# Kernel tuning notes

Hardware: AMD Instinct MI355X
Metric: run time of the kernel (lower is better)

## Reference

```python
import jax, jax.numpy as jnp
import numpy as np

EPS = 1e-6
ROPE_THETA = 10000.0


def rms_norm(x, w):
    # x: [..., hd]
    var = jnp.mean(x * x, axis=-1, keepdims=True)
    return x * jax.lax.rsqrt(var + EPS) * w


def apply_rope(x):
    # x: [B, L, nH, hd], rotate-half RoPE over sequence positions
    B, L, nH, hd = x.shape
    half = hd // 2
    inv_freq = 1.0 / (ROPE_THETA ** (jnp.arange(half, dtype=jnp.float32) / half))
    pos = jnp.arange(L, dtype=jnp.float32)
    freqs = pos[:, None] * inv_freq[None, :]          # [L, half]
    cos = jnp.cos(freqs)[None, :, None, :]            # [1, L, 1, half]
    sin = jnp.sin(freqs)[None, :, None, :]
    x1, x2 = x[..., :half], x[..., half:]
    return jnp.concatenate([x1 * cos - x2 * sin, x1 * sin + x2 * cos], axis=-1)


def setup_inputs() -> dict:
    key = jax.random.key(0)
    ks = jax.random.split(key, 5)
    B, H, W, C = 2, 48, 48, 512
    nH, nKV = 8, 4
    hd = C // nH
    s = 0.02
    return {
        "x": jax.random.normal(ks[0], (B, H, W, C), jnp.float32),
        "wq": jax.random.normal(ks[1], (C, C), jnp.float32) * s,
        "wk": jax.random.normal(ks[2], (C, nKV * hd), jnp.float32) * s,
        "wv": jax.random.normal(ks[3], (C, nKV * hd), jnp.float32) * s,
        "wo": jax.random.normal(ks[4], (C, C), jnp.float32) * s,
        "q_norm_w": jnp.ones((hd,), jnp.float32),
        "k_norm_w": jnp.ones((hd,), jnp.float32),
    }


def reference(x, wq, wk, wv, wo, q_norm_w, k_norm_w):
    B, H, W, C = x.shape
    L = H * W
    nH = 8
    hd = C // nH
    nKV = wk.shape[-1] // hd

    xf = x.reshape(B, L, C)
    q = (xf @ wq).reshape(B, L, nH, hd)
    k = (xf @ wk).reshape(B, L, nKV, hd)
    v = (xf @ wv).reshape(B, L, nKV, hd)

    q = apply_rope(rms_norm(q, q_norm_w))
    k = apply_rope(rms_norm(k, k_norm_w))

    q = q.transpose(0, 2, 1, 3)                       # [B, nH, L, hd]
    k = k.transpose(0, 2, 1, 3)                       # [B, nKV, L, hd]
    v = v.transpose(0, 2, 1, 3)
    if nKV < nH:
        rep = nH // nKV
        k = jnp.repeat(k, rep, axis=1)                # repeat_interleave over heads
        v = jnp.repeat(v, rep, axis=1)

    scale = 1.0 / jnp.sqrt(jnp.array(hd, jnp.float32))
    scores = jnp.einsum("bhqd,bhkd->bhqk", q, k) * scale
    attn = jax.nn.softmax(scores, axis=-1)
    out = jnp.einsum("bhqk,bhkd->bhqd", attn, v)      # [B, nH, L, hd]
    out = out.transpose(0, 2, 1, 3).reshape(B, H, W, C)
    return out @ wo
```

## Files before the change

### kernel.cpp

```cpp
#include <hip/hip_runtime.h>
#include <cstdint>
#include <cmath>

typedef float    f32x4  __attribute__((ext_vector_type(4)));
typedef uint32_t u32x4  __attribute__((ext_vector_type(4)));
typedef uint16_t u16x8  __attribute__((ext_vector_type(8)));
typedef __bf16   bf16x8 __attribute__((ext_vector_type(8)));

#define DEVI __device__ __forceinline__

#if __has_builtin(__builtin_amdgcn_exp2f)
DEVI float fast_exp2(float x) { return __builtin_amdgcn_exp2f(x); }
#else
DEVI float fast_exp2(float x) { return exp2f(x); }
#endif

constexpr int L   = 2304;
constexpr int C   = 512;
constexpr int NH  = 8;
constexpr int NKV = 4;
constexpr int HD  = 64;
constexpr int Bn  = 2;
constexpr int M   = Bn * L;
constexpr int NQKV = C + 2 * NKV * HD;
constexpr int NSPLIT = 4;
constexpr int KTILES = 36 / NSPLIT;

constexpr int LDA = 40;
constexpr int LDP = 72;

DEVI uint16_t f2bf(float f) {
  union { float f; uint32_t u; } v; v.f = f;
  uint32_t u = v.u;
  return (uint16_t)((u + 0x7fffu + ((u >> 16) & 1u)) >> 16);
}
DEVI float bf2f(uint16_t h) {
  union { uint32_t u; float f; } v; v.u = ((uint32_t)h) << 16;
  return v.f;
}
DEVI uint16_t f2h(float f) {
  _Float16 h = (_Float16)f;
  return __builtin_bit_cast(uint16_t, h);
}
DEVI float h2f(uint16_t u) {
  return (float)__builtin_bit_cast(_Float16, u);
}

DEVI bool detect_fp32(const void* qw_raw) {
  return ((const uint16_t*)qw_raw)[0] == 0;
}

DEVI f32x4 mfma_bf16(u32x4 a, u32x4 b, f32x4 c) {
  return __builtin_amdgcn_mfma_f32_16x16x32_bf16(
      __builtin_bit_cast(bf16x8, a), __builtin_bit_cast(bf16x8, b), c, 0, 0, 0);
}

DEVI void gld16(const void* g, void* l) {
  __builtin_amdgcn_global_load_lds((const __attribute__((address_space(1))) void*)g,
                                   (__attribute__((address_space(3))) void*)l,
                                   16, 0, 0);
}

__global__ __launch_bounds__(256) void k_prep(
    const void* __restrict__ x,
    const void* __restrict__ wq, const void* __restrict__ wk,
    const void* __restrict__ wv, const void* __restrict__ wo,
    const void* __restrict__ qw_raw,
    uint16_t* __restrict__ xb,
    uint16_t* __restrict__ wqkvT, uint16_t* __restrict__ woT) {
  const bool f32 = detect_fp32(qw_raw);
  const int bi = blockIdx.x;
  const int t = threadIdx.x;
  if (bi >= 192) {
    const int i = ((bi - 192) * 256 + t) * 8;
    if (f32) {
      const float* xf = (const float*)x;
      const f32x4 v0 = *(const f32x4*)&xf[i];
      const f32x4 v1 = *(const f32x4*)&xf[i + 4];
      u16x8 o;
#pragma unroll
      for (int j = 0; j < 4; ++j) { o[j] = f2bf(v0[j]); o[j + 4] = f2bf(v1[j]); }
      *(u16x8*)&xb[i] = o;
    } else {
      *(u16x8*)&xb[i] = *(const u16x8*)((const uint16_t*)x + i);
    }
    return;
  }
  __shared__ uint16_t tile[64][72];
  const void* src; uint16_t* dst;
  int src_ld, col0, n0, k0;
  if (bi < 128) {
    const int nt = bi & 15, kt = bi >> 4;
    n0 = nt * 64; k0 = kt * 64;
    if (n0 < 512)      { src = wq; src_ld = 512; col0 = n0; }
    else if (n0 < 768) { src = wk; src_ld = 256; col0 = n0 - 512; }
    else               { src = wv; src_ld = 256; col0 = n0 - 768; }
    dst = wqkvT + n0 * 512 + k0;
  } else {
    const int bi2 = bi - 128;
    const int nt = bi2 & 7, kt = bi2 >> 3;
    n0 = nt * 64; k0 = kt * 64;
    src = wo; src_ld = 512; col0 = n0;
    dst = woT + n0 * 512 + k0;
  }
  const int rr = t >> 2, c4 = t & 3;
  if (f32) {
    const float* s32 = (const float*)src;
    for (int cc = c4; cc < 8; cc += 4) {
      const f32x4 v0 = *(const f32x4*)&s32[(k0 + rr) * src_ld + col0 + cc * 8];
      const f32x4 v1 = *(const f32x4*)&s32[(k0 + rr) * src_ld + col0 + cc * 8 + 4];
      for (int j = 0; j < 4; ++j) {
        tile[rr][cc * 8 + j]     = f2bf(v0[j]);
        tile[rr][cc * 8 + j + 4] = f2bf(v1[j]);
      }
    }
  } else {
    const uint16_t* s16 = (const uint16_t*)src;
    for (int cc = c4; cc < 8; cc += 4) {
      const u16x8 v = *(const u16x8*)&s16[(k0 + rr) * src_ld + col0 + cc * 8];
      for (int j = 0; j < 8; ++j) tile[rr][cc * 8 + j] = v[j];
    }
  }
  __syncthreads();
  for (int cc = c4; cc < 8; cc += 4) {
    u16x8 o;
    for (int j = 0; j < 8; ++j) o[j] = tile[cc * 8 + j][rr];
    *(u16x8*)&dst[rr * 512 + cc * 8] = o;
  }
}

DEVI void gemm128_core(const uint16_t* __restrict__ A, const uint16_t* __restrict__ Bt,
                       int m0, int n0, uint16_t* As, uint16_t* Bs, f32x4 acc[4][4]) {
  const int t = threadIdx.x;
  const int lane = t & 63, wave = t >> 6;
  const int l15 = lane & 15, quad = lane >> 4;
  const int wm = wave >> 1, wn = wave & 1;
#pragma unroll
  for (int i = 0; i < 4; ++i)
#pragma unroll
    for (int j = 0; j < 4; ++j) acc[i][j] = f32x4{0.f, 0.f, 0.f, 0.f};

  const int r0 = t >> 2, c0 = t & 3;

  for (int k0 = 0; k0 < C; k0 += 32) {
    const u16x8 a0 = *(const u16x8*)&A [(m0 + r0)      * C + k0 + c0 * 8];
    const u16x8 a1 = *(const u16x8*)&A [(m0 + r0 + 64) * C + k0 + c0 * 8];
    const u16x8 b0 = *(const u16x8*)&Bt[(n0 + r0)      * C + k0 + c0 * 8];
    const u16x8 b1 = *(const u16x8*)&Bt[(n0 + r0 + 64) * C + k0 + c0 * 8];
    __syncthreads();
    *(u16x8*)&As[r0 * LDA + c0 * 8]        = a0;
    *(u16x8*)&As[(r0 + 64) * LDA + c0 * 8] = a1;
    *(u16x8*)&Bs[r0 * LDA + c0 * 8]        = b0;
    *(u16x8*)&Bs[(r0 + 64) * LDA + c0 * 8] = b1;
    __syncthreads();
    u32x4 af[4], bf[4];
#pragma unroll
    for (int mt = 0; mt < 4; ++mt)
      af[mt] = *(const u32x4*)&As[(wm * 64 + mt * 16 + l15) * LDA + quad * 8];
#pragma unroll
    for (int nt = 0; nt < 4; ++nt)
      bf[nt] = *(const u32x4*)&Bs[(wn * 64 + nt * 16 + l15) * LDA + quad * 8];
#pragma unroll
    for (int mt = 0; mt < 4; ++mt)
#pragma unroll
      for (int nt = 0; nt < 4; ++nt)
        acc[mt][nt] = mfma_bf16(af[mt], bf[nt], acc[mt][nt]);
  }
}

__global__ __launch_bounds__(256, 2) void k_gemm_qkv(
    const uint16_t* __restrict__ xb, const uint16_t* __restrict__ wqkvT,
    uint16_t* __restrict__ q_p, uint16_t* __restrict__ k_p, uint16_t* __restrict__ v_t,
    const void* __restrict__ qw_raw, const void* __restrict__ kw_raw) {
  __shared__ uint16_t As[128 * LDA], Bs[128 * LDA];
  const bool f32 = detect_fp32(qw_raw);
  const int m0 = blockIdx.x * 128, n0 = blockIdx.y * 128;
  f32x4 acc[4][4];
  gemm128_core(xb, wqkvT, m0, n0, As, Bs, acc);
  const int t = threadIdx.x, lane = t & 63, wave = t >> 6;
  const int l15 = lane & 15, quad = lane >> 4;
  const int wm = wave >> 1, wn = wave & 1;
  const int col0 = n0 + wn * 64;

  if (col0 < C + NKV * HD) {
    const bool isq = (col0 < C);
    const void* wr = isq ? qw_raw : kw_raw;
    float w4[4];
#pragma unroll
    for (int nt = 0; nt < 4; ++nt)
      w4[nt] = f32 ? ((const float*)wr)[nt * 16 + l15]
                   : bf2f(((const uint16_t*)wr)[nt * 16 + l15]);
    const float cfreq = -0.41524101186092f;
    const float f0 = fast_exp2((float)l15 * cfreq);
    const float f1 = fast_exp2((float)(16 + l15) * cfreq);
    float sF0, cF0, sF1, cF1;
    sincosf(f0, &sF0, &cF0);
    sincosf(f1, &sF1, &cF1);
    const float sc = isq ? 0.125f * 1.44269504088896f : 1.0f;
    const int head = isq ? (col0 >> 6) : ((col0 - C) >> 6);
    uint16_t* plane = isq ? q_p : k_p;
    const int nheads = isq ? NH : NKV;
#pragma unroll
    for (int mt = 0; mt < 4; ++mt) {
      const int gm = m0 + wm * 64 + mt * 16 + quad * 4;
      const int b = gm / L;
      const int l = gm - b * L;
      uint16_t* dst = plane + ((b * nheads + head) * L + l) * HD + l15;
      float s0, c0, s1, c1;
      sincosf((float)l * f0, &s0, &c0);
      sincosf((float)l * f1, &s1, &c1);
#pragma unroll
      for (int r = 0; r < 4; ++r) {
        float x0 = acc[mt][0][r], x1 = acc[mt][1][r];
        float x2 = acc[mt][2][r], x3 = acc[mt][3][r];
        float ss = x0 * x0 + x1 * x1 + x2 * x2 + x3 * x3;
        ss += __shfl_xor(ss, 1, 64); ss += __shfl_xor(ss, 2, 64);
        ss += __shfl_xor(ss, 4, 64); ss += __shfl_xor(ss, 8, 64);
        const float inv = 1.0f / sqrtf(ss * (1.0f / 64.0f) + 1e-6f);
        x0 *= inv * w4[0]; x1 *= inv * w4[1]; x2 *= inv * w4[2]; x3 *= inv * w4[3];
        dst[r * HD +  0] = f2bf((x0 * c0 - x2 * s0) * sc);
        dst[r * HD + 16] = f2bf((x1 * c1 - x3 * s1) * sc);
        dst[r * HD + 32] = f2bf((x0 * s0 + x2 * c0) * sc);
        dst[r * HD + 48] = f2bf((x1 * s1 + x3 * c1) * sc);
        const float ns0 = s0 * cF0 + c0 * sF0, nc0 = c0 * cF0 - s0 * sF0;
        const float ns1 = s1 * cF1 + c1 * sF1, nc1 = c1 * cF1 - s1 * sF1;
        s0 = ns0; c0 = nc0; s1 = ns1; c1 = nc1;
      }
    }
  } else {
    const int vh = (col0 - C - NKV * HD) >> 6;
#pragma unroll
    for (int mt = 0; mt < 4; ++mt) {
      const int gm = m0 + wm * 64 + mt * 16 + quad * 4;
      const int b = gm / L;
      const int l = gm - b * L;
#pragma unroll
      for (int nt = 0; nt < 4; ++nt) {
        uint16_t* dst = v_t + ((b * NKV + vh) * HD + nt * 16 + l15) * L + l;
#pragma unroll
        for (int r = 0; r < 4; ++r) dst[r] = f2bf(acc[mt][nt][r]);
      }
    }
  }
}

__global__ __launch_bounds__(256, 3) void k_attn(
    const uint16_t* __restrict__ q_p, const uint16_t* __restrict__ k_p,
    const uint16_t* __restrict__ v_t,
    uint16_t* __restrict__ Ohat, float* __restrict__ lpart) {
  __shared__ uint16_t Ks[2][4096], Vs[4096];
  __shared__ uint16_t Ps[4][48 * LDP];
  const int t = threadIdx.x, lane = t & 63, wave = t >> 6;
  const int l15 = lane & 15, quad = lane >> 4;

  const int bid = blockIdx.x;
  const int s   = bid / 192;
  const int rem = bid - s * 192;
  const int bkvh = rem / 24;
  const int qg   = rem - bkvh * 24;
  const int b = bkvh >> 2, kvh = bkvh & 3;
  const int u = qg * 4 + wave;
  const int h_local = u / 48;
  const int qt = u - h_local * 48;
  const int bh = b * NH + kvh * 2 + h_local;
  const int q0 = qt * 48;

  const uint16_t* qbase = q_p + (bh * L + q0) * HD;
  const uint16_t* kbase = k_p + (b * NKV + kvh) * L * HD;
  const uint16_t* vbase = v_t + (b * NKV + kvh) * HD * L;
  const int kstart = s * KTILES * 64;

  u32x4 qf[3][2];
#pragma unroll
  for (int mt = 0; mt < 3; ++mt)
#pragma unroll
    for (int ks = 0; ks < 2; ++ks)
      qf[mt][ks] = *(const u32x4*)&qbase[(mt * 16 + l15) * HD + (ks * 4 + quad) * 8];

  f32x4 O[3][4];
  float lp[3][4];
#pragma unroll
  for (int mt = 0; mt < 3; ++mt) {
#pragma unroll
    for (int nt = 0; nt < 4; ++nt) O[mt][nt] = f32x4{0.f, 0.f, 0.f, 0.f};
#pragma unroll
    for (int r = 0; r < 4; ++r) lp[mt][r] = 0.f;
  }

  uint16_t* Pw = Ps[wave];

  auto stageK = [&](int key0, int buf) {
#pragma unroll
    for (int rr = 0; rr < 2; ++rr) {
      const int slotbase = rr * 256 + wave * 64;
      const int slot = slotbase + lane;
      const int row = slot >> 3, cs = slot & 7;
      const int ch = cs ^ (row & 7);
      gld16(&kbase[(key0 + row) * HD + ch * 8], &Ks[buf][slotbase * 8]);
    }
  };
  auto stageV = [&](int key0) {
#pragma unroll
    for (int rr = 0; rr < 2; ++rr) {
      const int slotbase = rr * 256 + wave * 64;
      const int slot = slotbase + lane;
      const int row = slot >> 3, cs = slot & 7;
      const int ch = cs ^ (row & 7);
      gld16(&vbase[row * L + key0 + ch * 8], &Vs[slotbase * 8]);
    }
  };

  stageK(kstart, 0);

#pragma unroll 1
  for (int kb = 0; kb < KTILES; ++kb) {
    const int cur = kb & 1;
    __syncthreads();
    stageV(kstart + kb * 64);
    if (kb + 1 < KTILES) stageK(kstart + (kb + 1) * 64, cur ^ 1);

#pragma unroll
    for (int nt = 0; nt < 4; ++nt) {
      f32x4 S[3];
#pragma unroll
      for (int mt = 0; mt < 3; ++mt) S[mt] = f32x4{0.f, 0.f, 0.f, 0.f};
      const int kr = nt * 16 + l15;
#pragma unroll
      for (int ks = 0; ks < 2; ++ks) {
        const int ch = ks * 4 + quad;
        const u32x4 kf = *(const u32x4*)&Ks[cur][(kr * 8 + (ch ^ (kr & 7))) * 8];
#pragma unroll
        for (int mt = 0; mt < 3; ++mt)
          S[mt] = mfma_bf16(qf[mt][ks], kf, S[mt]);
      }
#pragma unroll
      for (int mt = 0; mt < 3; ++mt)
#pragma unroll
        for (int r = 0; r < 4; ++r) {
          const float p = fast_exp2(S[mt][r]);
          lp[mt][r] += p;
          Pw[(mt * 16 + quad * 4 + r) * LDP + nt * 16 + l15] = f2bf(p);
        }
    }

    __syncthreads();

#pragma unroll
    for (int ks = 0; ks < 2; ++ks) {
      const int ch = ks * 4 + quad;
      u32x4 pf[3];
#pragma unroll
      for (int mt = 0; mt < 3; ++mt)
        pf[mt] = *(const u32x4*)&Pw[(mt * 16 + l15) * LDP + ch * 8];
#pragma unroll
      for (int nt = 0; nt < 4; ++nt) {
        const int dr = nt * 16 + l15;
        const u32x4 vf = *(const u32x4*)&Vs[(dr * 8 + (ch ^ (dr & 7))) * 8];
#pragma unroll
        for (int mt = 0; mt < 3; ++mt)
          O[mt][nt] = mfma_bf16(pf[mt], vf, O[mt][nt]);
      }
    }
  }

  const int obase = (s * 16 + bh) * L + q0;
#pragma unroll
  for (int mt = 0; mt < 3; ++mt)
#pragma unroll
    for (int r = 0; r < 4; ++r) {
      float lv = lp[mt][r];
#pragma unroll
      for (int m = 1; m < 16; m <<= 1) lv += __shfl_xor(lv, m, 64);
      const float rl = 1.0f / lv;
      const int row = obase + mt * 16 + quad * 4 + r;
      if (l15 == 0) lpart[row] = lv;
#pragma unroll
      for (int nt = 0; nt < 4; ++nt)
        Ohat[row * HD + nt * 16 + l15] = f2h(O[mt][nt][r] * rl);
    }
}

__global__ __launch_bounds__(256) void k_combine(
    const uint16_t* __restrict__ Ohat, const float* __restrict__ lpart,
    uint16_t* __restrict__ attn) {
  const int idx = blockIdx.x * 256 + threadIdx.x;
  const int row = idx >> 6, d = idx & 63;
  float o = 0.f, l = 0.f;
#pragma unroll
  for (int s = 0; s < NSPLIT; ++s) {
    const float ls = lpart[s * 16 * L + row];
    o += h2f(Ohat[s * 16 * L * HD + idx]) * ls;
    l += ls;
  }
  const int bh = row / L, lq = row - bh * L;
  const int b = bh >> 3, h = bh & 7;
  attn[(b * L + lq) * C + h * HD + d] = f2bf(o / l);
}

__global__ __launch_bounds__(256, 2) void k_gemm_out(
    const uint16_t* __restrict__ attn, const uint16_t* __restrict__ woT,
    void* __restrict__ out, const void* __restrict__ qw_raw) {
  __shared__ uint16_t As[128 * LDA], Bs[128 * LDA];
  const bool f32 = detect_fp32(qw_raw);
  const int m0 = blockIdx.x * 128, n0 = blockIdx.y * 128;
  f32x4 acc[4][4];
  gemm128_core(attn, woT, m0, n0, As, Bs, acc);
  const int t = threadIdx.x, lane = t & 63, wave = t >> 6;
  const int l15 = lane & 15, quad = lane >> 4;
  const int wm = wave >> 1, wn = wave & 1;
#pragma unroll
  for (int mt = 0; mt < 4; ++mt) {
    const int gm = m0 + wm * 64 + mt * 16 + quad * 4;
#pragma unroll
    for (int nt = 0; nt < 4; ++nt) {
      const int gn = n0 + wn * 64 + nt * 16 + l15;
      if (f32) {
        float* o32 = (float*)out;
#pragma unroll
        for (int r = 0; r < 4; ++r) o32[(gm + r) * C + gn] = acc[mt][nt][r];
      } else {
        uint16_t* o16 = (uint16_t*)out;
#pragma unroll
        for (int r = 0; r < 4; ++r) o16[(gm + r) * C + gn] = f2bf(acc[mt][nt][r]);
      }
    }
  }
}

extern "C" void kernel_launch(void* const* d_in, const int* in_sizes, int n_in,
                              void* d_out, int out_size, void* d_ws, size_t ws_size,
                              hipStream_t stream) {
  const void* x  = d_in[0];
  const void* wq = d_in[1];
  const void* wk = d_in[2];
  const void* wv = d_in[3];
  const void* wo = d_in[4];
  const void* qw = d_in[5];
  const void* kw = d_in[6];

  uint16_t* ws = (uint16_t*)d_ws;
  uint16_t* xb    = ws;
  uint16_t* wqkvT = xb    + M * C;
  uint16_t* woT   = wqkvT + 1024 * 512;
  uint16_t* q_p   = woT   + 512 * 512;
  uint16_t* k_p   = q_p + Bn * NH  * L * HD;
  uint16_t* v_t   = k_p + Bn * NKV * L * HD;
  uint16_t* attn  = v_t + Bn * NKV * L * HD;
  uint16_t* Ohat  = attn + M * C;
  float*    lpart = (float*)(Ohat + NSPLIT * 16 * L * HD);

  k_prep      <<<dim3(192 + M * C / (256 * 8)), dim3(256), 0, stream>>>(
                  x, wq, wk, wv, wo, qw, xb, wqkvT, woT);
  k_gemm_qkv  <<<dim3(M / 128, NQKV / 128), dim3(256), 0, stream>>>(
                  xb, wqkvT, q_p, k_p, v_t, qw, kw);
  k_attn      <<<dim3(768), dim3(256), 0, stream>>>(q_p, k_p, v_t, Ohat, lpart);
  k_combine   <<<dim3(16 * L * HD / 256), dim3(256), 0, stream>>>(Ohat, lpart, attn);
  k_gemm_out  <<<dim3(M / 128, C / 128), dim3(256), 0, stream>>>(attn, woT, d_out, qw);
}
```

Before: 147.3 us.

## Use direct global-to-LDS loads with XOR swizzle, set MFMA priority, vectorize combine

New measurement: 139.7 us. -5.2%, faster.

```diff
diff --git a/kernel.cpp b/kernel.cpp
--- a/kernel.cpp
+++ b/kernel.cpp
@@ -26,7 +26,6 @@
 constexpr int NSPLIT = 4;
 constexpr int KTILES = 36 / NSPLIT;
 
-constexpr int LDA = 40;
 constexpr int LDP = 72;
 
 DEVI uint16_t f2bf(float f) {
@@ -140,31 +139,38 @@
 #pragma unroll
     for (int j = 0; j < 4; ++j) acc[i][j] = f32x4{0.f, 0.f, 0.f, 0.f};
 
-  const int r0 = t >> 2, c0 = t & 3;
-
-  for (int k0 = 0; k0 < C; k0 += 32) {
-    const u16x8 a0 = *(const u16x8*)&A [(m0 + r0)      * C + k0 + c0 * 8];
-    const u16x8 a1 = *(const u16x8*)&A [(m0 + r0 + 64) * C + k0 + c0 * 8];
-    const u16x8 b0 = *(const u16x8*)&Bt[(n0 + r0)      * C + k0 + c0 * 8];
-    const u16x8 b1 = *(const u16x8*)&Bt[(n0 + r0 + 64) * C + k0 + c0 * 8];
+  for (int k0 = 0; k0 < C; k0 += 64) {
     __syncthreads();
-    *(u16x8*)&As[r0 * LDA + c0 * 8]        = a0;
-    *(u16x8*)&As[(r0 + 64) * LDA + c0 * 8] = a1;
-    *(u16x8*)&Bs[r0 * LDA + c0 * 8]        = b0;
-    *(u16x8*)&Bs[(r0 + 64) * LDA + c0 * 8] = b1;
+#pragma unroll
+    for (int rr = 0; rr < 4; ++rr) {
+      const int slotbase = rr * 256 + wave * 64;
+      const int slot = slotbase + lane;
+      const int row = slot >> 3;
+      const int ch = (slot & 7) ^ (row & 7);
+      gld16(&A [(m0 + row) * C + k0 + ch * 8], &As[slotbase * 8]);
+      gld16(&Bt[(n0 + row) * C + k0 + ch * 8], &Bs[slotbase * 8]);
+    }
     __syncthreads();
-    u32x4 af[4], bf[4];
-#pragma unroll
-    for (int mt = 0; mt < 4; ++mt)
-      af[mt] = *(const u32x4*)&As[(wm * 64 + mt * 16 + l15) * LDA + quad * 8];
-#pragma unroll
-    for (int nt = 0; nt < 4; ++nt)
-      bf[nt] = *(const u32x4*)&Bs[(wn * 64 + nt * 16 + l15) * LDA + quad * 8];
-#pragma unroll
-    for (int mt = 0; mt < 4; ++mt)
-#pragma unroll
-      for (int nt = 0; nt < 4; ++nt)
-        acc[mt][nt] = mfma_bf16(af[mt], bf[nt], acc[mt][nt]);
+#pragma unroll
+    for (int ks = 0; ks < 2; ++ks) {
+      const int c = ks * 4 + quad;
+      u32x4 af[4], bf[4];
+#pragma unroll
+      for (int mt = 0; mt < 4; ++mt) {
+        const int r = wm * 64 + mt * 16 + l15;
+        af[mt] = *(const u32x4*)&As[r * 64 + (c ^ (r & 7)) * 8];
+      }
+#pragma unroll
+      for (int nt = 0; nt < 4; ++nt) {
+        const int r = wn * 64 + nt * 16 + l15;
+        bf[nt] = *(const u32x4*)&Bs[r * 64 + (c ^ (r & 7)) * 8];
+      }
+#pragma unroll
+      for (int mt = 0; mt < 4; ++mt)
+#pragma unroll
+        for (int nt = 0; nt < 4; ++nt)
+          acc[mt][nt] = mfma_bf16(af[mt], bf[nt], acc[mt][nt]);
+    }
   }
 }
 
@@ -172,7 +178,7 @@
     const uint16_t* __restrict__ xb, const uint16_t* __restrict__ wqkvT,
     uint16_t* __restrict__ q_p, uint16_t* __restrict__ k_p, uint16_t* __restrict__ v_t,
     const void* __restrict__ qw_raw, const void* __restrict__ kw_raw) {
-  __shared__ uint16_t As[128 * LDA], Bs[128 * LDA];
+  __shared__ uint16_t As[128 * 64], Bs[128 * 64];
   const bool f32 = detect_fp32(qw_raw);
   const int m0 = blockIdx.x * 128, n0 = blockIdx.y * 128;
   f32x4 acc[4][4];
@@ -329,9 +335,11 @@
       for (int ks = 0; ks < 2; ++ks) {
         const int ch = ks * 4 + quad;
         const u32x4 kf = *(const u32x4*)&Ks[cur][(kr * 8 + (ch ^ (kr & 7))) * 8];
+        __builtin_amdgcn_s_setprio(1);
 #pragma unroll
         for (int mt = 0; mt < 3; ++mt)
           S[mt] = mfma_bf16(qf[mt][ks], kf, S[mt]);
+        __builtin_amdgcn_s_setprio(0);
       }
 #pragma unroll
       for (int mt = 0; mt < 3; ++mt)
@@ -356,9 +364,11 @@
       for (int nt = 0; nt < 4; ++nt) {
         const int dr = nt * 16 + l15;
         const u32x4 vf = *(const u32x4*)&Vs[(dr * 8 + (ch ^ (dr & 7))) * 8];
+        __builtin_amdgcn_s_setprio(1);
 #pragma unroll
         for (int mt = 0; mt < 3; ++mt)
           O[mt][nt] = mfma_bf16(pf[mt], vf, O[mt][nt]);
+        __builtin_amdgcn_s_setprio(0);
       }
     }
   }
@@ -383,24 +393,31 @@
 __global__ __launch_bounds__(256) void k_combine(
     const uint16_t* __restrict__ Ohat, const float* __restrict__ lpart,
     uint16_t* __restrict__ attn) {
-  const int idx = blockIdx.x * 256 + threadIdx.x;
-  const int row = idx >> 6, d = idx & 63;
-  float o = 0.f, l = 0.f;
+  const int idx8 = blockIdx.x * 256 + threadIdx.x;
+  const int row = idx8 >> 3, d0 = (idx8 & 7) * 8;
+  float o[8] = {0.f, 0.f, 0.f, 0.f, 0.f, 0.f, 0.f, 0.f};
+  float l = 0.f;
 #pragma unroll
   for (int s = 0; s < NSPLIT; ++s) {
     const float ls = lpart[s * 16 * L + row];
-    o += h2f(Ohat[s * 16 * L * HD + idx]) * ls;
+    const u16x8 v = *(const u16x8*)&Ohat[(s * 16 * L + row) * HD + d0];
+#pragma unroll
+    for (int j = 0; j < 8; ++j) o[j] += h2f(v[j]) * ls;
     l += ls;
   }
   const int bh = row / L, lq = row - bh * L;
   const int b = bh >> 3, h = bh & 7;
-  attn[(b * L + lq) * C + h * HD + d] = f2bf(o / l);
+  const float rl = 1.0f / l;
+  u16x8 ov;
+#pragma unroll
+  for (int j = 0; j < 8; ++j) ov[j] = f2bf(o[j] * rl);
+  *(u16x8*)&attn[(b * L + lq) * C + h * HD + d0] = ov;
 }
 
 __global__ __launch_bounds__(256, 2) void k_gemm_out(
     const uint16_t* __restrict__ attn, const uint16_t* __restrict__ woT,
     void* __restrict__ out, const void* __restrict__ qw_raw) {
-  __shared__ uint16_t As[128 * LDA], Bs[128 * LDA];
+  __shared__ uint16_t As[128 * 64], Bs[128 * 64];
   const bool f32 = detect_fp32(qw_raw);
   const int m0 = blockIdx.x * 128, n0 = blockIdx.y * 128;
   f32x4 acc[4][4];
@@ -454,6 +471,6 @@
   k_gemm_qkv  <<<dim3(M / 128, NQKV / 128), dim3(256), 0, stream>>>(
                   xb, wqkvT, q_p, k_p, v_t, qw, kw);
   k_attn      <<<dim3(768), dim3(256), 0, stream>>>(q_p, k_p, v_t, Ohat, lpart);
-  k_combine   <<<dim3(16 * L * HD / 256), dim3(256), 0, stream>>>(Ohat, lpart, attn);
+  k_combine   <<<dim3(16 * L * HD / (256 * 8)), dim3(256), 0, stream>>>(Ohat, lpart, attn);
   k_gemm_out  <<<dim3(M / 128, C / 128), dim3(256), 0, stream>>>(attn, woT, d_out, qw);
 }
```
